# Optimization experiments

Hardware: AMD Instinct MI355X
Metric: run time of the kernel (lower is better)

Reference implementation:

```python
import jax, jax.numpy as jnp
import numpy as np

N_NODES = 100000
IN_CH, HIDDEN, OUT_CH = 128, 128, 64
N_POS, N_NEG = 600000, 600000


def _glorot(key, shape):
    lim = float(np.sqrt(6.0 / (shape[0] + shape[1])))
    return jax.random.uniform(key, shape, jnp.float32, -lim, lim)


def setup_inputs() -> dict:
    key = jax.random.key(0)
    k = jax.random.split(key, 7)
    x = jax.random.normal(k[0], (N_NODES, IN_CH), jnp.float32)
    pos_edge_index = jax.random.randint(k[1], (2, N_POS), 0, N_NODES, jnp.int64)
    neg_edge_index = jax.random.randint(k[2], (2, N_NEG), 0, N_NODES, jnp.int64)
    W1 = _glorot(k[3], (IN_CH, HIDDEN))
    b1 = jnp.zeros((HIDDEN,), jnp.float32)
    W2 = _glorot(k[4], (HIDDEN, OUT_CH))
    b2 = jnp.zeros((OUT_CH,), jnp.float32)
    return {"x": x, "pos_edge_index": pos_edge_index, "neg_edge_index": neg_edge_index,
            "W1": W1, "b1": b1, "W2": W2, "b2": b2}


def gcn_conv(x, W, b, src, dst, n_nodes):
    # PyG GCNConv: add self-loops, symmetric deg^-1/2 normalization, linear, bias
    h = x @ W                                               # [N, F_out]
    ones = jnp.ones(src.shape, h.dtype)
    deg = jax.ops.segment_sum(ones, dst, num_segments=n_nodes) + 1.0  # self-loop
    dinv = jax.lax.rsqrt(deg)                               # deg^-0.5, deg >= 1
    norm = dinv[src] * dinv[dst]                            # per-edge norm
    agg = jax.ops.segment_sum(h[src] * norm[:, None], dst, num_segments=n_nodes)
    agg = agg + h * (dinv * dinv)[:, None]                  # self-loop messages
    return agg + b


def reference(x, pos_edge_index, neg_edge_index, W1, b1, W2, b2):
    n = x.shape[0]
    src, dst = pos_edge_index[0], pos_edge_index[1]
    z = gcn_conv(x, W1, b1, src, dst, n)
    z = jax.nn.relu(z)
    z = gcn_conv(z, W2, b2, src, dst, n)
    # decode: gather endpoints of pos+neg edges, elementwise product, sum over feat
    ei = jnp.concatenate([pos_edge_index, neg_edge_index], axis=-1)  # [2, E_pos+E_neg]
    return jnp.sum(z[ei[0]] * z[ei[1]], axis=-1)
```

## Files before the change

kernel.cpp:

```cpp
#include <hip/hip_runtime.h>

#define N_NODES 100000
#define IN_CH 128
#define HIDDEN 128
#define OUT_CH 64
#define N_POS 600000
#define N_NEG 600000

typedef unsigned int uint32;
typedef unsigned short ushort16;
typedef __attribute__((ext_vector_type(8))) short bf16x8;
typedef __attribute__((ext_vector_type(4))) float f32x4;

__device__ inline float bf_lo(uint32 u) {
    union { uint32 i; float f; } v;
    v.i = u << 16;
    return v.f;
}
__device__ inline float bf_hi(uint32 u) {
    union { uint32 i; float f; } v;
    v.i = u & 0xffff0000u;
    return v.f;
}
__device__ inline ushort16 f2bf(float f) {
    union { uint32 i; float f; } v;
    v.f = f;
    uint32 r = v.i + 0x7fffu + ((v.i >> 16) & 1u);
    return (ushort16)(r >> 16);
}
__device__ inline uint32 pack2bf(float a, float b) {
    return (uint32)f2bf(a) | ((uint32)f2bf(b) << 16);
}

#define NB_HIST ((N_POS + 255) / 256)
#define NB_FILL ((N_POS + 255) / 256)
#define NB_GEMM1 ((N_NODES + 63) / 64)

__global__ void hist_wt(const int* __restrict__ dst, int* __restrict__ hist,
                        const float* __restrict__ W1, const float* __restrict__ W2,
                        ushort16* __restrict__ W1t, ushort16* __restrict__ W2t) {
    if (blockIdx.x < NB_HIST) {
        int i = blockIdx.x * 256 + threadIdx.x;
        if (i < N_POS) atomicAdd(&hist[dst[i]], 1);
    } else {
        int i = (blockIdx.x - NB_HIST) * 256 + threadIdx.x;
        if (i < 128 * 128) {
            int n = i >> 7, k = i & 127;
            W1t[i] = f2bf(W1[k * 128 + n]);
        } else {
            int j = i - 128 * 128;
            if (j < 64 * 128) {
                int n = j >> 7, k = j & 127;
                W2t[j] = f2bf(W2[k * 64 + n]);
            }
        }
    }
}

__global__ void scan_reduce(const int* __restrict__ hist, int* __restrict__ partials, int n) {
    __shared__ int sdata[256];
    int b = blockIdx.x, t = threadIdx.x;
    int base = b * 1024;
    int s = 0;
    for (int i = t; i < 1024; i += 256) {
        int idx = base + i;
        s += (idx < n) ? hist[idx] : 0;
    }
    sdata[t] = s;
    __syncthreads();
    for (int off = 128; off > 0; off >>= 1) {
        if (t < off) sdata[t] += sdata[t + off];
        __syncthreads();
    }
    if (t == 0) partials[b] = sdata[0];
}

__global__ void scan_final(const int* __restrict__ hist, const int* __restrict__ partials,
                           int* __restrict__ rowstart, int* __restrict__ cursor,
                           float* __restrict__ dinv, int n) {
    __shared__ int tsum[256];
    __shared__ int base_sh;
    int t = threadIdx.x, b = blockIdx.x;
    if (t < 64) {
        int s0 = (t < b) ? partials[t] : 0;
        int i2 = t + 64;
        int s1 = (i2 < b && i2 < 98) ? partials[i2] : 0;
        int s = s0 + s1;
#pragma unroll
        for (int off = 32; off > 0; off >>= 1) s += __shfl_down(s, off, 64);
        if (t == 0) base_sh = s;
    }
    int base = b * 1024 + t * 4;
    int v[4];
    int s = 0;
#pragma unroll
    for (int j = 0; j < 4; j++) {
        int i = base + j;
        v[j] = (i < n) ? hist[i] : 0;
        s += v[j];
    }
    tsum[t] = s;
    __syncthreads();
    for (int off = 1; off < 256; off <<= 1) {
        int a = (t >= off) ? tsum[t - off] : 0;
        __syncthreads();
        tsum[t] += a;
        __syncthreads();
    }
    int offset = base_sh + (tsum[t] - s);
#pragma unroll
    for (int j = 0; j < 4; j++) {
        int i = base + j;
        if (i < n) {
            rowstart[i] = offset;
            cursor[i] = offset;
            dinv[i] = rsqrtf((float)v[j] + 1.0f);
            offset += v[j];
        }
    }
    if (b == 0 && t == 0) rowstart[n] = N_POS;
}

template <int M, bool XBF>
__device__ __forceinline__ void gemm_tile(const void* __restrict__ Xv,
                                          const ushort16* __restrict__ Wt,
                                          ushort16* __restrict__ H, int n, int tileIdx) {
    constexpr int K = 128;
    constexpr int TN = 64;
    constexpr int KH = 64;
    constexpr int XS = 72;
    __shared__ short Xs[TN * XS];
    __shared__ short Ws[M * XS];
    int tid = threadIdx.x;
    int node0 = tileIdx * TN;

    constexpr int CT = M / 16;
    int w = tid >> 6;
    int lane = tid & 63;
    int l15 = lane & 15;
    int quad = lane >> 4;
    f32x4 acc[CT] = {};

#pragma unroll
    for (int h = 0; h < 2; ++h) {
        if (h) __syncthreads();
        for (int q = tid; q < M * 8; q += 256) {
            int row = q >> 3, c = q & 7;
            uint4 v = *(const uint4*)((const short*)Wt + row * K + h * KH + c * 8);
            *(uint4*)(Ws + row * XS + c * 8) = v;
        }
        if (!XBF) {
            const float* X = (const float*)Xv;
            int row = tid >> 2, part = tid & 3;
            int gn = node0 + row;
#pragma unroll
            for (int c = 0; c < 4; ++c) {
                int kl = part * 16 + c * 4;
                float4 v = (gn < n) ? *(const float4*)(X + (size_t)gn * K + h * KH + kl)
                                    : float4{0, 0, 0, 0};
                uint2 p = {pack2bf(v.x, v.y), pack2bf(v.z, v.w)};
                *(uint2*)(Xs + row * XS + kl) = p;
            }
        } else {
            const short* X = (const short*)Xv;
            for (int q = tid; q < TN * 8; q += 256) {
                int row = q >> 3, c = q & 7;
                int gn = node0 + row;
                uint4 v = (gn < n) ? *(const uint4*)(X + (size_t)gn * K + h * KH + c * 8)
                                   : uint4{0, 0, 0, 0};
                *(uint4*)(Xs + row * XS + c * 8) = v;
            }
        }
        __syncthreads();

        const short* xrow = Xs + (w * 16 + l15) * XS + quad * 8;
#pragma unroll
        for (int kk = 0; kk < 2; ++kk) {
            bf16x8 a = *(const bf16x8*)(xrow + kk * 32);
#pragma unroll
            for (int ct = 0; ct < CT; ++ct) {
                bf16x8 b = *(const bf16x8*)(Ws + (ct * 16 + l15) * XS + quad * 8 + kk * 32);
                acc[ct] = __builtin_amdgcn_mfma_f32_16x16x32_bf16(a, b, acc[ct], 0, 0, 0);
            }
        }
    }

#pragma unroll
    for (int ct = 0; ct < CT; ++ct) {
#pragma unroll
        for (int r = 0; r < 4; ++r) {
            int gn = node0 + w * 16 + quad * 4 + r;
            if (gn < n) H[(size_t)gn * M + ct * 16 + l15] = f2bf(acc[ct][r]);
        }
    }
}

__global__ __launch_bounds__(256) void csr_gemm1(
    const int* __restrict__ src, const int* __restrict__ dst, const float* __restrict__ dinv,
    int* __restrict__ cursor, int2* __restrict__ adjw, const float* __restrict__ x,
    const ushort16* __restrict__ W1t, ushort16* __restrict__ H, int n) {
    if (blockIdx.x < NB_FILL) {
        int e = blockIdx.x * 256 + threadIdx.x;
        if (e < N_POS) {
            int s = src[e], d = dst[e];
            int p = atomicAdd(&cursor[d], 1);
            adjw[p] = int2{s, __float_as_int(dinv[s] * dinv[d])};
        }
    } else {
        gemm_tile<HIDDEN, false>(x, W1t, H, n, blockIdx.x - NB_FILL);
    }
}

template <int M, bool XBF>
__global__ __launch_bounds__(256) void gemm_mfma(const void* __restrict__ Xv,
                                                 const ushort16* __restrict__ Wt,
                                                 ushort16* __restrict__ H, int n) {
    gemm_tile<M, XBF>(Xv, Wt, H, n, blockIdx.x);
}

template <int F, bool RELU>
__global__ void agg_pull(const int* __restrict__ rowstart, const int2* __restrict__ adjw,
                         const float* __restrict__ dinv, const ushort16* __restrict__ H,
                         const float* __restrict__ bias, ushort16* __restrict__ Z, int n) {
    int g = threadIdx.x >> 4;
    int l = threadIdx.x & 15;
    int node = blockIdx.x * (blockDim.x >> 4) + g;
    if (node >= n) return;
    float dn = dinv[node];
    int rs = rowstart[node], re = rowstart[node + 1];
    int deg = re - rs;
    int pc = (deg > 0) ? rs : (rs > 0 ? rs - 1 : 0);
    if (F == 128) {
        uint4 h[8];
        float wv[8];
#pragma unroll
        for (int j = 0; j < 8; ++j) {
            int p = (rs + j < re) ? rs + j : pc;
            int2 e = adjw[p];
            h[j] = *(const uint4*)(H + (size_t)e.x * F + l * 8);
            wv[j] = (j < deg) ? __int_as_float(e.y) : 0.0f;
        }
        float s0[8] = {}, s1[8] = {};
#pragma unroll
        for (int j = 0; j < 8; j += 2) {
            s0[0] += bf_lo(h[j].x) * wv[j]; s0[1] += bf_hi(h[j].x) * wv[j];
            s0[2] += bf_lo(h[j].y) * wv[j]; s0[3] += bf_hi(h[j].y) * wv[j];
            s0[4] += bf_lo(h[j].z) * wv[j]; s0[5] += bf_hi(h[j].z) * wv[j];
            s0[6] += bf_lo(h[j].w) * wv[j]; s0[7] += bf_hi(h[j].w) * wv[j];
            s1[0] += bf_lo(h[j + 1].x) * wv[j + 1]; s1[1] += bf_hi(h[j + 1].x) * wv[j + 1];
            s1[2] += bf_lo(h[j + 1].y) * wv[j + 1]; s1[3] += bf_hi(h[j + 1].y) * wv[j + 1];
            s1[4] += bf_lo(h[j + 1].z) * wv[j + 1]; s1[5] += bf_hi(h[j + 1].z) * wv[j + 1];
            s1[6] += bf_lo(h[j + 1].w) * wv[j + 1]; s1[7] += bf_hi(h[j + 1].w) * wv[j + 1];
        }
        for (int p = rs + 8; p < re; ++p) {
            int2 e = adjw[p];
            float w = __int_as_float(e.y);
            uint4 hh = *(const uint4*)(H + (size_t)e.x * F + l * 8);
            s0[0] += bf_lo(hh.x) * w; s0[1] += bf_hi(hh.x) * w;
            s0[2] += bf_lo(hh.y) * w; s0[3] += bf_hi(hh.y) * w;
            s0[4] += bf_lo(hh.z) * w; s0[5] += bf_hi(hh.z) * w;
            s0[6] += bf_lo(hh.w) * w; s0[7] += bf_hi(hh.w) * w;
        }
        uint4 hv = *(const uint4*)(H + (size_t)node * F + l * 8);
        float4 bv0 = *(const float4*)(bias + l * 8);
        float4 bv1 = *(const float4*)(bias + l * 8 + 4);
        float d2 = dn * dn;
        float hs[8] = {bf_lo(hv.x), bf_hi(hv.x), bf_lo(hv.y), bf_hi(hv.y),
                       bf_lo(hv.z), bf_hi(hv.z), bf_lo(hv.w), bf_hi(hv.w)};
        float bb[8] = {bv0.x, bv0.y, bv0.z, bv0.w, bv1.x, bv1.y, bv1.z, bv1.w};
        float v[8];
#pragma unroll
        for (int j = 0; j < 8; ++j) {
            v[j] = s0[j] + s1[j] + hs[j] * d2 + bb[j];
            if (RELU) v[j] = fmaxf(v[j], 0.0f);
        }
        *(uint4*)(Z + (size_t)node * F + l * 8) =
            uint4{pack2bf(v[0], v[1]), pack2bf(v[2], v[3]), pack2bf(v[4], v[5]),
                  pack2bf(v[6], v[7])};
    } else {
        uint2 h[8];
        float wv[8];
#pragma unroll
        for (int j = 0; j < 8; ++j) {
            int p = (rs + j < re) ? rs + j : pc;
            int2 e = adjw[p];
            h[j] = *(const uint2*)(H + (size_t)e.x * F + l * 4);
            wv[j] = (j < deg) ? __int_as_float(e.y) : 0.0f;
        }
        float s0[4] = {}, s1[4] = {};
#pragma unroll
        for (int j = 0; j < 8; j += 2) {
            s0[0] += bf_lo(h[j].x) * wv[j]; s0[1] += bf_hi(h[j].x) * wv[j];
            s0[2] += bf_lo(h[j].y) * wv[j]; s0[3] += bf_hi(h[j].y) * wv[j];
            s1[0] += bf_lo(h[j + 1].x) * wv[j + 1]; s1[1] += bf_hi(h[j + 1].x) * wv[j + 1];
            s1[2] += bf_lo(h[j + 1].y) * wv[j + 1]; s1[3] += bf_hi(h[j + 1].y) * wv[j + 1];
        }
        for (int p = rs + 8; p < re; ++p) {
            int2 e = adjw[p];
            float w = __int_as_float(e.y);
            uint2 hh = *(const uint2*)(H + (size_t)e.x * F + l * 4);
            s0[0] += bf_lo(hh.x) * w; s0[1] += bf_hi(hh.x) * w;
            s0[2] += bf_lo(hh.y) * w; s0[3] += bf_hi(hh.y) * w;
        }
        uint2 hv = *(const uint2*)(H + (size_t)node * F + l * 4);
        float4 bv = *(const float4*)(bias + l * 4);
        float d2 = dn * dn;
        float hs[4] = {bf_lo(hv.x), bf_hi(hv.x), bf_lo(hv.y), bf_hi(hv.y)};
        float bb[4] = {bv.x, bv.y, bv.z, bv.w};
        float v[4];
#pragma unroll
        for (int j = 0; j < 4; ++j) {
            v[j] = s0[j] + s1[j] + hs[j] * d2 + bb[j];
            if (RELU) v[j] = fmaxf(v[j], 0.0f);
        }
        *(uint2*)(Z + (size_t)node * F + l * 4) = uint2{pack2bf(v[0], v[1]), pack2bf(v[2], v[3])};
    }
}

__global__ void decode_mfma(const int* __restrict__ pos, const int* __restrict__ neg,
                            const short* __restrict__ Z, float* __restrict__ out) {
    int wid = threadIdx.x >> 6;
    int lane = threadIdx.x & 63;
    int l15 = lane & 15;
    int quad = lane >> 4;
    int e0 = (blockIdx.x * 4 + wid) * 32;
    if (e0 >= N_POS + N_NEG) return;
    const int* bp = (e0 < N_POS) ? pos : (neg - N_POS);
    int eA = e0 + l15;
    int eB = e0 + 16 + l15;
    int aA = bp[eA], bA = bp[600000 + eA];
    int aB = bp[eB], bB = bp[600000 + eB];

    const short* zaA = Z + (size_t)aA * OUT_CH + quad * 8;
    const short* zbA = Z + (size_t)bA * OUT_CH + quad * 8;
    const short* zaB = Z + (size_t)aB * OUT_CH + quad * 8;
    const short* zbB = Z + (size_t)bB * OUT_CH + quad * 8;
    bf16x8 a0A = *(const bf16x8*)(zaA);
    bf16x8 a1A = *(const bf16x8*)(zaA + 32);
    bf16x8 b0A = *(const bf16x8*)(zbA);
    bf16x8 b1A = *(const bf16x8*)(zbA + 32);
    bf16x8 a0B = *(const bf16x8*)(zaB);
    bf16x8 a1B = *(const bf16x8*)(zaB + 32);
    bf16x8 b0B = *(const bf16x8*)(zbB);
    bf16x8 b1B = *(const bf16x8*)(zbB + 32);

    f32x4 accA = {}, accB = {};
    accA = __builtin_amdgcn_mfma_f32_16x16x32_bf16(a0A, b0A, accA, 0, 0, 0);
    accB = __builtin_amdgcn_mfma_f32_16x16x32_bf16(a0B, b0B, accB, 0, 0, 0);
    accA = __builtin_amdgcn_mfma_f32_16x16x32_bf16(a1A, b1A, accA, 0, 0, 0);
    accB = __builtin_amdgcn_mfma_f32_16x16x32_bf16(a1B, b1B, accB, 0, 0, 0);

    if (quad == (l15 >> 2)) {
        out[eA] = accA[l15 & 3];
        out[eB] = accB[l15 & 3];
    }
}

extern "C" void kernel_launch(void* const* d_in, const int* in_sizes, int n_in,
                              void* d_out, int out_size, void* d_ws, size_t ws_size,
                              hipStream_t stream) {
    const float* x = (const float*)d_in[0];
    const int* pos = (const int*)d_in[1];
    const int* neg = (const int*)d_in[2];
    const float* W1 = (const float*)d_in[3];
    const float* b1 = (const float*)d_in[4];
    const float* W2 = (const float*)d_in[5];
    const float* b2 = (const float*)d_in[6];
    float* out = (float*)d_out;

    ushort16* A = (ushort16*)d_ws;
    ushort16* B = A + (size_t)N_NODES * 128;
    float* dinv = (float*)(B + (size_t)N_NODES * 128);
    int* hist = (int*)(dinv + N_NODES);
    int* rowstart = hist + N_NODES;
    int* cursor = rowstart + N_NODES + 1;
    int2* adjw = (int2*)(cursor + N_NODES);
    int* partials = (int*)(adjw + N_POS);
    ushort16* W1t = (ushort16*)(partials + 128);
    ushort16* W2t = W1t + 128 * 128;

    const int* pos_src = pos;
    const int* pos_dst = pos + N_POS;

    constexpr int NB_SCAN = (N_NODES + 1023) / 1024;

    hipMemsetAsync(hist, 0, N_NODES * sizeof(int), stream);
    hist_wt<<<NB_HIST + 96, 256, 0, stream>>>(pos_dst, hist, W1, W2, W1t, W2t);
    scan_reduce<<<NB_SCAN, 256, 0, stream>>>(hist, partials, N_NODES);
    scan_final<<<NB_SCAN, 256, 0, stream>>>(hist, partials, rowstart, cursor, dinv, N_NODES);

    csr_gemm1<<<NB_FILL + NB_GEMM1, 256, 0, stream>>>(pos_src, pos_dst, dinv, cursor, adjw, x,
                                                      W1t, A, N_NODES);

    agg_pull<HIDDEN, true><<<(N_NODES + 15) / 16, 256, 0, stream>>>(rowstart, adjw, dinv, A, b1,
                                                                    B, N_NODES);

    ushort16* h2 = A;
    gemm_mfma<OUT_CH, true><<<(N_NODES + 63) / 64, 256, 0, stream>>>(B, W2t, h2, N_NODES);
    ushort16* z2 = B;
    agg_pull<OUT_CH, false><<<(N_NODES + 15) / 16, 256, 0, stream>>>(rowstart, adjw, dinv, h2, b2,
                                                                     z2, N_NODES);

    decode_mfma<<<(N_POS + N_NEG) / 128, 256, 0, stream>>>(pos, neg, (const short*)z2, out);
}
```

Baseline: 270.4 us.

## Fuse layer-1 aggregation with layer-2 GEMM and vectorize edge histogram/fill

The layer-1 pull aggregation now writes its ReLU'd bf16 rows into shared memory, and the same block runs the 64-wide MFMA GEMM against W2 staged in LDS. This removes one kernel launch and the global write and read of the 100k x 128 intermediate. The histogram and CSR fill kernels now read four edges per thread with int4 loads. The fused kernel needs more LDS and registers, and its aggregation uses only 64 nodes per block, which may lower occupancy.

```diff
diff --git a/kernel.cpp b/kernel.cpp
--- a/kernel.cpp
+++ b/kernel.cpp
@@ -32,18 +32,24 @@
     return (uint32)f2bf(a) | ((uint32)f2bf(b) << 16);
 }
 
-#define NB_HIST ((N_POS + 255) / 256)
-#define NB_FILL ((N_POS + 255) / 256)
+#define NB_HIST4 ((N_POS / 4 + 255) / 256)
+#define NB_FILL4 ((N_POS / 4 + 255) / 256)
 #define NB_GEMM1 ((N_NODES + 63) / 64)
 
 __global__ void hist_wt(const int* __restrict__ dst, int* __restrict__ hist,
                         const float* __restrict__ W1, const float* __restrict__ W2,
                         ushort16* __restrict__ W1t, ushort16* __restrict__ W2t) {
-    if (blockIdx.x < NB_HIST) {
-        int i = blockIdx.x * 256 + threadIdx.x;
-        if (i < N_POS) atomicAdd(&hist[dst[i]], 1);
+    if (blockIdx.x < NB_HIST4) {
+        int e = (blockIdx.x * 256 + threadIdx.x) * 4;
+        if (e < N_POS) {
+            int4 d4 = *(const int4*)(dst + e);
+            atomicAdd(&hist[d4.x], 1);
+            atomicAdd(&hist[d4.y], 1);
+            atomicAdd(&hist[d4.z], 1);
+            atomicAdd(&hist[d4.w], 1);
+        }
     } else {
-        int i = (blockIdx.x - NB_HIST) * 256 + threadIdx.x;
+        int i = (blockIdx.x - NB_HIST4) * 256 + threadIdx.x;
         if (i < 128 * 128) {
             int n = i >> 7, k = i & 127;
             W1t[i] = f2bf(W1[k * 128 + n]);
@@ -199,23 +205,130 @@
     const int* __restrict__ src, const int* __restrict__ dst, const float* __restrict__ dinv,
     int* __restrict__ cursor, int2* __restrict__ adjw, const float* __restrict__ x,
     const ushort16* __restrict__ W1t, ushort16* __restrict__ H, int n) {
-    if (blockIdx.x < NB_FILL) {
-        int e = blockIdx.x * 256 + threadIdx.x;
+    if (blockIdx.x < NB_FILL4) {
+        int e = (blockIdx.x * 256 + threadIdx.x) * 4;
         if (e < N_POS) {
-            int s = src[e], d = dst[e];
-            int p = atomicAdd(&cursor[d], 1);
-            adjw[p] = int2{s, __float_as_int(dinv[s] * dinv[d])};
+            int4 s4 = *(const int4*)(src + e);
+            int4 d4 = *(const int4*)(dst + e);
+            float a0 = dinv[s4.x], a1 = dinv[s4.y], a2 = dinv[s4.z], a3 = dinv[s4.w];
+            float c0 = dinv[d4.x], c1 = dinv[d4.y], c2 = dinv[d4.z], c3 = dinv[d4.w];
+            int p0 = atomicAdd(&cursor[d4.x], 1);
+            int p1 = atomicAdd(&cursor[d4.y], 1);
+            int p2 = atomicAdd(&cursor[d4.z], 1);
+            int p3 = atomicAdd(&cursor[d4.w], 1);
+            adjw[p0] = int2{s4.x, __float_as_int(a0 * c0)};
+            adjw[p1] = int2{s4.y, __float_as_int(a1 * c1)};
+            adjw[p2] = int2{s4.z, __float_as_int(a2 * c2)};
+            adjw[p3] = int2{s4.w, __float_as_int(a3 * c3)};
         }
     } else {
-        gemm_tile<HIDDEN, false>(x, W1t, H, n, blockIdx.x - NB_FILL);
-    }
-}
-
-template <int M, bool XBF>
-__global__ __launch_bounds__(256) void gemm_mfma(const void* __restrict__ Xv,
-                                                 const ushort16* __restrict__ Wt,
-                                                 ushort16* __restrict__ H, int n) {
-    gemm_tile<M, XBF>(Xv, Wt, H, n, blockIdx.x);
+        gemm_tile<HIDDEN, false>(x, W1t, H, n, blockIdx.x - NB_FILL4);
+    }
+}
+
+__device__ __forceinline__ uint4 agg_node128(int node, int l, const int* __restrict__ rowstart,
+                                             const int2* __restrict__ adjw,
+                                             const float* __restrict__ dinv,
+                                             const ushort16* __restrict__ H,
+                                             const float* __restrict__ bias) {
+    float dn = dinv[node];
+    int rs = rowstart[node], re = rowstart[node + 1];
+    int deg = re - rs;
+    int pc = (deg > 0) ? rs : (rs > 0 ? rs - 1 : 0);
+    uint4 h[8];
+    float wv[8];
+#pragma unroll
+    for (int j = 0; j < 8; ++j) {
+        int p = (rs + j < re) ? rs + j : pc;
+        int2 e = adjw[p];
+        h[j] = *(const uint4*)(H + (size_t)e.x * 128 + l * 8);
+        wv[j] = (j < deg) ? __int_as_float(e.y) : 0.0f;
+    }
+    float s0[8] = {}, s1[8] = {};
+#pragma unroll
+    for (int j = 0; j < 8; j += 2) {
+        s0[0] += bf_lo(h[j].x) * wv[j]; s0[1] += bf_hi(h[j].x) * wv[j];
+        s0[2] += bf_lo(h[j].y) * wv[j]; s0[3] += bf_hi(h[j].y) * wv[j];
+        s0[4] += bf_lo(h[j].z) * wv[j]; s0[5] += bf_hi(h[j].z) * wv[j];
+        s0[6] += bf_lo(h[j].w) * wv[j]; s0[7] += bf_hi(h[j].w) * wv[j];
+        s1[0] += bf_lo(h[j + 1].x) * wv[j + 1]; s1[1] += bf_hi(h[j + 1].x) * wv[j + 1];
+        s1[2] += bf_lo(h[j + 1].y) * wv[j + 1]; s1[3] += bf_hi(h[j + 1].y) * wv[j + 1];
+        s1[4] += bf_lo(h[j + 1].z) * wv[j + 1]; s1[5] += bf_hi(h[j + 1].z) * wv[j + 1];
+        s1[6] += bf_lo(h[j + 1].w) * wv[j + 1]; s1[7] += bf_hi(h[j + 1].w) * wv[j + 1];
+    }
+    for (int p = rs + 8; p < re; ++p) {
+        int2 e = adjw[p];
+        float w = __int_as_float(e.y);
+        uint4 hh = *(const uint4*)(H + (size_t)e.x * 128 + l * 8);
+        s0[0] += bf_lo(hh.x) * w; s0[1] += bf_hi(hh.x) * w;
+        s0[2] += bf_lo(hh.y) * w; s0[3] += bf_hi(hh.y) * w;
+        s0[4] += bf_lo(hh.z) * w; s0[5] += bf_hi(hh.z) * w;
+        s0[6] += bf_lo(hh.w) * w; s0[7] += bf_hi(hh.w) * w;
+    }
+    uint4 hv = *(const uint4*)(H + (size_t)node * 128 + l * 8);
+    float4 bv0 = *(const float4*)(bias + l * 8);
+    float4 bv1 = *(const float4*)(bias + l * 8 + 4);
+    float d2 = dn * dn;
+    float hs[8] = {bf_lo(hv.x), bf_hi(hv.x), bf_lo(hv.y), bf_hi(hv.y),
+                   bf_lo(hv.z), bf_hi(hv.z), bf_lo(hv.w), bf_hi(hv.w)};
+    float bb[8] = {bv0.x, bv0.y, bv0.z, bv0.w, bv1.x, bv1.y, bv1.z, bv1.w};
+    float v[8];
+#pragma unroll
+    for (int j = 0; j < 8; ++j) {
+        v[j] = fmaxf(s0[j] + s1[j] + hs[j] * d2 + bb[j], 0.0f);
+    }
+    return uint4{pack2bf(v[0], v[1]), pack2bf(v[2], v[3]), pack2bf(v[4], v[5]),
+                 pack2bf(v[6], v[7])};
+}
+
+#define ZS 136
+__global__ __launch_bounds__(256, 4) void agg1_gemm2(
+    const int* __restrict__ rowstart, const int2* __restrict__ adjw,
+    const float* __restrict__ dinv, const ushort16* __restrict__ H,
+    const float* __restrict__ b1, const ushort16* __restrict__ W2t,
+    ushort16* __restrict__ h2, int n) {
+    __shared__ __align__(16) short Zs[64 * ZS];
+    __shared__ __align__(16) short Ws[64 * ZS];
+    int tid = threadIdx.x;
+    int node0 = blockIdx.x * 64;
+
+    for (int q = tid; q < 64 * 16; q += 256) {
+        int row = q >> 4, c = q & 15;
+        uint4 v = *(const uint4*)((const short*)W2t + row * 128 + c * 8);
+        *(uint4*)(Ws + row * ZS + c * 8) = v;
+    }
+
+    int g = tid >> 4, l = tid & 15;
+#pragma unroll 1
+    for (int it = 0; it < 4; ++it) {
+        int row = g * 4 + it;
+        int node = node0 + row;
+        uint4 z = (node < n) ? agg_node128(node, l, rowstart, adjw, dinv, H, b1)
+                             : uint4{0, 0, 0, 0};
+        *(uint4*)(Zs + row * ZS + l * 8) = z;
+    }
+    __syncthreads();
+
+    int w = tid >> 6, lane = tid & 63, l15 = lane & 15, quad = lane >> 4;
+    f32x4 acc[4] = {};
+    const short* zrow = Zs + (w * 16 + l15) * ZS + quad * 8;
+#pragma unroll
+    for (int kk = 0; kk < 4; ++kk) {
+        bf16x8 a = *(const bf16x8*)(zrow + kk * 32);
+#pragma unroll
+        for (int ct = 0; ct < 4; ++ct) {
+            bf16x8 b = *(const bf16x8*)(Ws + (ct * 16 + l15) * ZS + quad * 8 + kk * 32);
+            acc[ct] = __builtin_amdgcn_mfma_f32_16x16x32_bf16(a, b, acc[ct], 0, 0, 0);
+        }
+    }
+#pragma unroll
+    for (int ct = 0; ct < 4; ++ct) {
+#pragma unroll
+        for (int r = 0; r < 4; ++r) {
+            int gn = node0 + w * 16 + quad * 4 + r;
+            if (gn < n) h2[(size_t)gn * OUT_CH + ct * 16 + l15] = f2bf(acc[ct][r]);
+        }
+    }
 }
 
 template <int F, bool RELU>
@@ -385,21 +498,18 @@
     constexpr int NB_SCAN = (N_NODES + 1023) / 1024;
 
     hipMemsetAsync(hist, 0, N_NODES * sizeof(int), stream);
-    hist_wt<<<NB_HIST + 96, 256, 0, stream>>>(pos_dst, hist, W1, W2, W1t, W2t);
+    hist_wt<<<NB_HIST4 + 96, 256, 0, stream>>>(pos_dst, hist, W1, W2, W1t, W2t);
     scan_reduce<<<NB_SCAN, 256, 0, stream>>>(hist, partials, N_NODES);
     scan_final<<<NB_SCAN, 256, 0, stream>>>(hist, partials, rowstart, cursor, dinv, N_NODES);
 
-    csr_gemm1<<<NB_FILL + NB_GEMM1, 256, 0, stream>>>(pos_src, pos_dst, dinv, cursor, adjw, x,
-                                                      W1t, A, N_NODES);
-
-    agg_pull<HIDDEN, true><<<(N_NODES + 15) / 16, 256, 0, stream>>>(rowstart, adjw, dinv, A, b1,
-                                                                    B, N_NODES);
-
-    ushort16* h2 = A;
-    gemm_mfma<OUT_CH, true><<<(N_NODES + 63) / 64, 256, 0, stream>>>(B, W2t, h2, N_NODES);
-    ushort16* z2 = B;
-    agg_pull<OUT_CH, false><<<(N_NODES + 15) / 16, 256, 0, stream>>>(rowstart, adjw, dinv, h2, b2,
-                                                                     z2, N_NODES);
-
-    decode_mfma<<<(N_POS + N_NEG) / 128, 256, 0, stream>>>(pos, neg, (const short*)z2, out);
-}
+    csr_gemm1<<<NB_FILL4 + NB_GEMM1, 256, 0, stream>>>(pos_src, pos_dst, dinv, cursor, adjw, x,
+                                                       W1t, A, N_NODES);
+
+    agg1_gemm2<<<(N_NODES + 63) / 64, 256, 0, stream>>>(rowstart, adjw, dinv, A, b1, W2t, B,
+                                                        N_NODES);
+
+    agg_pull<OUT_CH, false><<<(N_NODES + 15) / 16, 256, 0, stream>>>(rowstart, adjw, dinv, B, b2,
+                                                                     A, N_NODES);
+
+    decode_mfma<<<(N_POS + N_NEG) / 128, 256, 0, stream>>>(pos, neg, (const short*)A, out);
+}
```

Result: slower. 275.9 us (+2.0%).
